# Performance work log

Hardware: AMD Instinct MI355X
Metric: run time of the kernel (lower is better)

The kernel has to match this reference:

```python
import jax, jax.numpy as jnp
import numpy as np

EMBED = 1024
HEADS = 16
HEAD_DIM = EMBED // HEADS
MAX_REL = 16


def setup_inputs() -> dict:
    key = jax.random.key(0)
    ks = jax.random.split(key, 8)
    s = 0.02
    x = jax.random.normal(ks[0], (4, 2048, EMBED), dtype=jnp.float32)
    Wq = jax.random.normal(ks[1], (EMBED, EMBED), dtype=jnp.float32) * s
    bq = jnp.zeros((EMBED,), dtype=jnp.float32)
    Wk = jax.random.normal(ks[2], (EMBED, EMBED), dtype=jnp.float32) * s
    bk = jnp.zeros((EMBED,), dtype=jnp.float32)
    Wv = jax.random.normal(ks[3], (EMBED, EMBED), dtype=jnp.float32) * s
    bv = jnp.zeros((EMBED,), dtype=jnp.float32)
    rel_bias = jax.random.normal(ks[4], (2 * MAX_REL + 1, HEADS), dtype=jnp.float32) * s
    return {"x": x, "Wq": Wq, "bq": bq, "Wk": Wk, "bk": bk, "Wv": Wv, "bv": bv, "rel_bias": rel_bias}


def reference(x, Wq, bq, Wk, bk, Wv, bv, rel_bias):
    B, S, _ = x.shape
    # projections (Linear: x @ W + b, with W stored [in, out])
    q = (x @ Wq + bq).reshape(B, S, HEADS, HEAD_DIM).transpose(0, 2, 1, 3)  # [B,H,S,D]
    k = (x @ Wk + bk).reshape(B, S, HEADS, HEAD_DIM).transpose(0, 2, 1, 3)
    v = (x @ Wv + bv).reshape(B, S, HEADS, HEAD_DIM).transpose(0, 2, 1, 3)
    scores = jnp.einsum('bhqd,bhkd->bhqk', q, k) / jnp.sqrt(jnp.float32(HEAD_DIM))
    pos = jnp.arange(S)
    rel = jnp.clip(pos[None, :] - pos[:, None], -MAX_REL, MAX_REL) + MAX_REL  # [S,S]
    bias = rel_bias[rel]                      # [S,S,H]
    scores = scores + bias.transpose(2, 0, 1)[None]  # [B,H,S,S]
    probs = jax.nn.softmax(scores, axis=-1)
    # dropout is identity in eval mode
    out = jnp.einsum('bhqk,bhkd->bhqd', probs, v)
    return out.transpose(0, 2, 1, 3).reshape(B, S, EMBED)
```

## Files before the change

### kernel.cpp

```cpp
#include <hip/hip_runtime.h>

#define EMBED 1024
#define HEADS 16
#define HDIM  64
#define SEQ   2048
#define BATCH 4
#define MTOT  (BATCH*SEQ)

typedef __attribute__((ext_vector_type(8))) short  short8;
typedef __attribute__((ext_vector_type(4))) float  f32x4;

#define GLOAD_LDS16(g, l) \
  __builtin_amdgcn_global_load_lds((const __attribute__((address_space(1))) void*)(g), \
                                   (__attribute__((address_space(3))) void*)(l), 16, 0, 0)

__device__ inline unsigned short f2bf(float f) {
  union { float f; unsigned u; } v; v.f = f;
  unsigned r = v.u + 0x7FFF + ((v.u >> 16) & 1);
  return (unsigned short)(r >> 16);
}

__global__ void cvt_x(const float* __restrict__ x, unsigned short* __restrict__ xb) {
  int i = (blockIdx.x * blockDim.x + threadIdx.x) * 8;
  f32x4 a = *(const f32x4*)(x + i);
  f32x4 b = *(const f32x4*)(x + i + 4);
  unsigned short o[8];
  o[0]=f2bf(a[0]); o[1]=f2bf(a[1]); o[2]=f2bf(a[2]); o[3]=f2bf(a[3]);
  o[4]=f2bf(b[0]); o[5]=f2bf(b[1]); o[6]=f2bf(b[2]); o[7]=f2bf(b[3]);
  *(short8*)(xb + i) = *(short8*)o;
}

__global__ void transpose_w(const float* __restrict__ Wq, const float* __restrict__ Wk,
                            const float* __restrict__ Wv, unsigned short* __restrict__ Wtb) {
  __shared__ float tile[32][33];
  int wsel = blockIdx.z;
  const float* W = wsel == 0 ? Wq : (wsel == 1 ? Wk : Wv);
  int k0 = blockIdx.x * 32, n0 = blockIdx.y * 32;
  int tx = threadIdx.x & 31, ty = threadIdx.x >> 5;
  for (int i = 0; i < 4; ++i)
    tile[ty + i*8][tx] = W[(k0 + ty + i*8) * EMBED + n0 + tx];
  __syncthreads();
  unsigned short* o = Wtb + wsel * EMBED * EMBED;
  for (int i = 0; i < 4; ++i)
    o[(n0 + ty + i*8) * EMBED + k0 + tx] = f2bf(tile[tx][ty + i*8]);
}

__global__ __launch_bounds__(256)
void qkv_gemm(const unsigned short* __restrict__ xb, const unsigned short* __restrict__ Wtb,
              const float* __restrict__ bq, const float* __restrict__ bk, const float* __restrict__ bv,
              unsigned short* __restrict__ Qb, unsigned short* __restrict__ Kb,
              unsigned short* __restrict__ Vt) {
  __shared__ unsigned short As[128 * 72];
  __shared__ unsigned short Bs[128 * 72];
  int wsel = blockIdx.z;
  int m0 = blockIdx.x * 128, n0 = blockIdx.y * 128;
  int t = threadIdx.x, lane = t & 63, wave = t >> 6;
  int wr = wave >> 1, wc = wave & 1;
  int lr = lane & 15, lg = lane >> 4;
  const unsigned short* Wt = Wtb + wsel * (EMBED * EMBED);
  const float* bias = wsel == 0 ? bq : (wsel == 1 ? bk : bv);

  f32x4 acc[4][4] = {};

  for (int kt = 0; kt < EMBED / 64; ++kt) {
    int k0 = kt * 64;
    for (int i = 0; i < 4; ++i) {
      int c = i * 256 + t;
      int row = c >> 3, col8 = c & 7;
      short8 va = *(const short8*)(xb + (m0 + row) * EMBED + k0 + col8 * 8);
      short8 vb = *(const short8*)(Wt + (n0 + row) * EMBED + k0 + col8 * 8);
      *(short8*)(As + row * 72 + col8 * 8) = va;
      *(short8*)(Bs + row * 72 + col8 * 8) = vb;
    }
    __syncthreads();
    for (int kk = 0; kk < 2; ++kk) {
      short8 af[4], bfr[4];
      for (int mf = 0; mf < 4; ++mf)
        af[mf] = *(const short8*)(As + (wr * 64 + mf * 16 + lr) * 72 + kk * 32 + lg * 8);
      for (int nf = 0; nf < 4; ++nf)
        bfr[nf] = *(const short8*)(Bs + (wc * 64 + nf * 16 + lr) * 72 + kk * 32 + lg * 8);
      for (int mf = 0; mf < 4; ++mf)
        for (int nf = 0; nf < 4; ++nf)
          acc[mf][nf] = __builtin_amdgcn_mfma_f32_16x16x32_bf16(af[mf], bfr[nf], acc[mf][nf], 0, 0, 0);
    }
    __syncthreads();
  }

  for (int nf = 0; nf < 4; ++nf) {
    int n = n0 + wc * 64 + nf * 16 + lr;
    float bval = bias[n];
    int h = n >> 6, d = n & 63;
    for (int mf = 0; mf < 4; ++mf) {
      for (int r = 0; r < 4; ++r) {
        int m = m0 + wr * 64 + mf * 16 + lg * 4 + r;
        int b = m >> 11, s = m & 2047;
        unsigned short bfv = f2bf(acc[mf][nf][r] + bval);
        if (wsel == 0)      Qb[((b * HEADS + h) * SEQ + s) * HDIM + d] = bfv;
        else if (wsel == 1) Kb[((b * HEADS + h) * SEQ + s) * HDIM + d] = bfv;
        else                Vt[((b * HEADS + h) * HDIM + d) * SEQ + s] = bfv;
      }
    }
  }
}

__global__ __launch_bounds__(256)
void attn(const unsigned short* __restrict__ Qb, const unsigned short* __restrict__ Kb,
          const unsigned short* __restrict__ Vt, const float* __restrict__ rel_bias,
          float* __restrict__ out) {
  __shared__ unsigned short Ks[2][64 * 64];
  __shared__ unsigned short Vs[2][64 * 64];
  __shared__ unsigned short Plds[4][16 * 80];
  __shared__ float bias_l[33];
  int bh = blockIdx.y;
  int b = bh >> 4, h = bh & 15;
  int t = threadIdx.x, lane = t & 63, wave = t >> 6;
  int lr = lane & 15, lg = lane >> 4;
  const float LOG2E = 1.44269504088896340736f;
  if (t < 33) bias_l[t] = rel_bias[t * HEADS + h] * LOG2E;

  int q0 = blockIdx.x * 64 + wave * 16;
  const unsigned short* Qp = Qb + (bh * SEQ + q0) * HDIM;
  const unsigned short* Kp = Kb + bh * SEQ * HDIM;
  const unsigned short* Vp = Vt + bh * HDIM * SEQ;

  short8 qf[2];
  for (int kk = 0; kk < 2; ++kk)
    qf[kk] = *(const short8*)(Qp + lr * HDIM + kk * 32 + lg * 8);

  f32x4 oacc[4] = {};
  float lsum[4] = {0.f, 0.f, 0.f, 0.f};
  const float SCL = 0.125f * LOG2E;
  unsigned short* pw = Plds[wave];

  int srow0 = (wave << 4) + (lane >> 3);
  int sslot = lane & 7;

  #define STAGE(buf, key0_)                                                          \
    for (int j = 0; j < 2; ++j) {                                                    \
      int srow = srow0 + j * 8;                                                      \
      int cs = sslot ^ (srow & 7);                                                   \
      GLOAD_LDS16(Kp + ((key0_) + srow) * HDIM + cs * 8,                             \
                  &Ks[buf][((wave << 4) + j * 8) << 6]);                             \
      GLOAD_LDS16(Vp + srow * SEQ + (key0_) + cs * 8,                                \
                  &Vs[buf][((wave << 4) + j * 8) << 6]);                             \
    }

  int cur = 0;
  STAGE(0, 0)
  __syncthreads();
  float cbLo = bias_l[0], cbHi = bias_l[32];

  for (int kb = 0; kb < SEQ / 64; ++kb) {
    int key0 = kb * 64;
    if (kb + 1 < SEQ / 64) { STAGE(cur ^ 1, key0 + 64) }
    f32x4 sc[4] = {};
    for (int kf = 0; kf < 4; ++kf) {
      int row = kf * 16 + lr;
      for (int kk = 0; kk < 2; ++kk) {
        short8 kfr = *(const short8*)(&Ks[cur][(row << 6) + (((kk * 4 + lg) ^ (row & 7)) << 3)]);
        sc[kf] = __builtin_amdgcn_mfma_f32_16x16x32_bf16(qf[kk], kfr, sc[kf], 0, 0, 0);
      }
    }
    float p[4][4];
    if (key0 >= q0 + 31) {
      for (int kf = 0; kf < 4; ++kf)
        for (int r = 0; r < 4; ++r)
          p[kf][r] = exp2f(sc[kf][r] * SCL + cbHi);
    } else if (key0 <= q0 - 79) {
      for (int kf = 0; kf < 4; ++kf)
        for (int r = 0; r < 4; ++r)
          p[kf][r] = exp2f(sc[kf][r] * SCL + cbLo);
    } else {
      for (int kf = 0; kf < 4; ++kf) {
        int key = key0 + kf * 16 + lr;
        for (int r = 0; r < 4; ++r) {
          int q = q0 + lg * 4 + r;
          int rel = key - q;
          rel = rel < -16 ? -16 : (rel > 16 ? 16 : rel);
          p[kf][r] = exp2f(sc[kf][r] * SCL + bias_l[rel + 16]);
        }
      }
    }
    for (int r = 0; r < 4; ++r)
      lsum[r] += p[0][r] + p[1][r] + p[2][r] + p[3][r];
    for (int kf = 0; kf < 4; ++kf)
      for (int r = 0; r < 4; ++r)
        pw[(lg * 4 + r) * 80 + kf * 16 + lr] = f2bf(p[kf][r]);
    short8 pa[2];
    for (int kk = 0; kk < 2; ++kk)
      pa[kk] = *(const short8*)(pw + lr * 80 + kk * 32 + lg * 8);
    for (int df = 0; df < 4; ++df) {
      int row = df * 16 + lr;
      for (int kk = 0; kk < 2; ++kk) {
        short8 vf = *(const short8*)(&Vs[cur][(row << 6) + (((kk * 4 + lg) ^ (row & 7)) << 3)]);
        oacc[df] = __builtin_amdgcn_mfma_f32_16x16x32_bf16(pa[kk], vf, oacc[df], 0, 0, 0);
      }
    }
    __syncthreads();
    cur ^= 1;
  }
  for (int r = 0; r < 4; ++r) {
    float s_ = lsum[r];
    for (int off = 1; off < 16; off <<= 1)
      s_ += __shfl_xor(s_, off, 64);
    int q = q0 + lg * 4 + r;
    float inv = 1.0f / s_;
    float* op = out + (b * SEQ + q) * EMBED + h * HDIM;
    for (int df = 0; df < 4; ++df)
      op[df * 16 + lr] = oacc[df][r] * inv;
  }
  #undef STAGE
}

extern "C" void kernel_launch(void* const* d_in, const int* in_sizes, int n_in,
                              void* d_out, int out_size, void* d_ws, size_t ws_size,
                              hipStream_t stream) {
  const float* x        = (const float*)d_in[0];
  const float* Wq       = (const float*)d_in[1];
  const float* bq       = (const float*)d_in[2];
  const float* Wk       = (const float*)d_in[3];
  const float* bk       = (const float*)d_in[4];
  const float* Wv       = (const float*)d_in[5];
  const float* bv       = (const float*)d_in[6];
  const float* rel_bias = (const float*)d_in[7];
  float* out = (float*)d_out;

  char* ws = (char*)d_ws;
  unsigned short* xb  = (unsigned short*)(ws);
  unsigned short* Wtb = (unsigned short*)(ws + 16777216);
  unsigned short* Qb  = (unsigned short*)(ws + 23068672);
  unsigned short* Kb  = (unsigned short*)(ws + 39845888);
  unsigned short* Vt  = (unsigned short*)(ws + 56623104);

  cvt_x<<<MTOT * EMBED / (256 * 8), 256, 0, stream>>>(x, xb);
  transpose_w<<<dim3(32, 32, 3), 256, 0, stream>>>(Wq, Wk, Wv, Wtb);
  qkv_gemm<<<dim3(MTOT / 128, EMBED / 128, 3), 256, 0, stream>>>(xb, Wtb, bq, bk, bv, Qb, Kb, Vt);
  attn<<<dim3(SEQ / 64, BATCH * HEADS), 256, 0, stream>>>(Qb, Kb, Vt, rel_bias, out);
}
```

Measured before the change: 243.4 us.

## Switch attention to 32x32 MFMA with register-resident P via permlane swaps

The attention kernel now gives each wave 32 queries and computes S transposed with 32x32x16 bf16 MFMAs. Converted probabilities are repacked in registers using v_cvt_pk_bf16 and v_permlane32_swap, so P no longer round-trips through LDS. Each block covers 128 queries, which halves the grid and doubles reuse of each staged K/V tile. This trades fewer blocks and higher register pressure (two 16-float accumulators plus scores) for less LDS traffic and fewer MFMA instructions.

```diff
diff --git a/kernel.cpp b/kernel.cpp
--- a/kernel.cpp
+++ b/kernel.cpp
@@ -7,8 +7,9 @@
 #define BATCH 4
 #define MTOT  (BATCH*SEQ)
 
-typedef __attribute__((ext_vector_type(8))) short  short8;
-typedef __attribute__((ext_vector_type(4))) float  f32x4;
+typedef __attribute__((ext_vector_type(8)))  short short8;
+typedef __attribute__((ext_vector_type(4)))  float f32x4;
+typedef __attribute__((ext_vector_type(16))) float f32x16;
 
 #define GLOAD_LDS16(g, l) \
   __builtin_amdgcn_global_load_lds((const __attribute__((address_space(1))) void*)(g), \
@@ -18,6 +19,20 @@
   union { float f; unsigned u; } v; v.f = f;
   unsigned r = v.u + 0x7FFF + ((v.u >> 16) & 1);
   return (unsigned short)(r >> 16);
+}
+
+__device__ inline unsigned cvtpk(float lo, float hi) {
+  unsigned r;
+  asm("v_cvt_pk_bf16_f32 %0, %1, %2" : "=v"(r) : "v"(lo), "v"(hi));
+  return r;
+}
+
+#define PLSWAP(a, b) asm("v_permlane32_swap_b32 %0, %1" : "+v"(a), "+v"(b))
+
+__device__ inline short8 mk8(unsigned w0, unsigned w1, unsigned w2, unsigned w3) {
+  union { unsigned u[4]; short8 s; } x;
+  x.u[0] = w0; x.u[1] = w1; x.u[2] = w2; x.u[3] = w3;
+  return x.s;
 }
 
 __global__ void cvt_x(const float* __restrict__ x, unsigned short* __restrict__ xb) {
@@ -109,28 +124,29 @@
           float* __restrict__ out) {
   __shared__ unsigned short Ks[2][64 * 64];
   __shared__ unsigned short Vs[2][64 * 64];
-  __shared__ unsigned short Plds[4][16 * 80];
   __shared__ float bias_l[33];
+  __shared__ float dld[4][32];
   int bh = blockIdx.y;
   int b = bh >> 4, h = bh & 15;
   int t = threadIdx.x, lane = t & 63, wave = t >> 6;
-  int lr = lane & 15, lg = lane >> 4;
+  int l31 = lane & 31, hi = lane >> 5;
   const float LOG2E = 1.44269504088896340736f;
   if (t < 33) bias_l[t] = rel_bias[t * HEADS + h] * LOG2E;
 
-  int q0 = blockIdx.x * 64 + wave * 16;
-  const unsigned short* Qp = Qb + (bh * SEQ + q0) * HDIM;
+  int qw0 = blockIdx.x * 128 + wave * 32;
+  const unsigned short* Qp = Qb + (bh * SEQ + qw0) * HDIM;
   const unsigned short* Kp = Kb + bh * SEQ * HDIM;
   const unsigned short* Vp = Vt + bh * HDIM * SEQ;
 
-  short8 qf[2];
-  for (int kk = 0; kk < 2; ++kk)
-    qf[kk] = *(const short8*)(Qp + lr * HDIM + kk * 32 + lg * 8);
-
-  f32x4 oacc[4] = {};
-  float lsum[4] = {0.f, 0.f, 0.f, 0.f};
+  short8 qf[4];
+  #pragma unroll
+  for (int ks = 0; ks < 4; ++ks)
+    qf[ks] = *(const short8*)(Qp + l31 * HDIM + ks * 16 + hi * 8);
+
+  f32x16 O0 = {}, O1 = {};
+  float lsum = 0.f;
   const float SCL = 0.125f * LOG2E;
-  unsigned short* pw = Plds[wave];
+  int q = qw0 + l31;
 
   int srow0 = (wave << 4) + (lane >> 3);
   int sslot = lane & 7;
@@ -150,66 +166,72 @@
   __syncthreads();
   float cbLo = bias_l[0], cbHi = bias_l[32];
 
+  #define LDV(row, ks) \
+    (*(const short8*)(&Vs[cur][((row) << 6) + ((((ks) * 2 + hi) ^ ((row) & 7)) << 3)]))
+
+  #define PROC(SACC, KOFF)  {                                                        \
+    float pv[16];                                                                    \
+    int kbase = key0 + (KOFF);                                                       \
+    if (kbase >= qw0 + 47) {                                                         \
+      _Pragma("unroll") for (int r = 0; r < 16; ++r)                                 \
+        pv[r] = exp2f(SACC[r] * SCL + cbHi);                                         \
+    } else if (kbase <= qw0 - 47) {                                                  \
+      _Pragma("unroll") for (int r = 0; r < 16; ++r)                                 \
+        pv[r] = exp2f(SACC[r] * SCL + cbLo);                                         \
+    } else {                                                                         \
+      _Pragma("unroll") for (int r = 0; r < 16; ++r) {                               \
+        int key = kbase + (r & 3) + 8 * (r >> 2) + 4 * hi;                           \
+        int rel = key - q;                                                           \
+        rel = rel < -16 ? -16 : (rel > 16 ? 16 : rel);                               \
+        pv[r] = exp2f(SACC[r] * SCL + bias_l[rel + 16]);                             \
+      }                                                                              \
+    }                                                                                \
+    _Pragma("unroll") for (int r = 0; r < 16; ++r) lsum += pv[r];                    \
+                       \
+    unsigned a0 = cvtpk(pv[0], pv[1]),  a1 = cvtpk(pv[4], pv[5]);   PLSWAP(a0, a1);  \
+    unsigned a2 = cvtpk(pv[2], pv[3]),  a3 = cvtpk(pv[6], pv[7]);   PLSWAP(a2, a3);  \
+    unsigned b0 = cvtpk(pv[8], pv[9]),  b1 = cvtpk(pv[12], pv[13]); PLSWAP(b0, b1);  \
+    unsigned b2 = cvtpk(pv[10], pv[11]), b3 = cvtpk(pv[14], pv[15]); PLSWAP(b2, b3); \
+    short8 pa0 = mk8(a0, a2, a1, a3);                                                \
+    short8 pa1 = mk8(b0, b2, b1, b3);                                                \
+    int ks0 = (KOFF) / 16;                                                           \
+    O0 = __builtin_amdgcn_mfma_f32_32x32x16_bf16(pa0, LDV(l31, ks0),      O0, 0, 0, 0); \
+    O1 = __builtin_amdgcn_mfma_f32_32x32x16_bf16(pa0, LDV(32 + l31, ks0), O1, 0, 0, 0); \
+    O0 = __builtin_amdgcn_mfma_f32_32x32x16_bf16(pa1, LDV(l31, ks0 + 1),      O0, 0, 0, 0); \
+    O1 = __builtin_amdgcn_mfma_f32_32x32x16_bf16(pa1, LDV(32 + l31, ks0 + 1), O1, 0, 0, 0); \
+  }
+
   for (int kb = 0; kb < SEQ / 64; ++kb) {
     int key0 = kb * 64;
     if (kb + 1 < SEQ / 64) { STAGE(cur ^ 1, key0 + 64) }
-    f32x4 sc[4] = {};
-    for (int kf = 0; kf < 4; ++kf) {
-      int row = kf * 16 + lr;
-      for (int kk = 0; kk < 2; ++kk) {
-        short8 kfr = *(const short8*)(&Ks[cur][(row << 6) + (((kk * 4 + lg) ^ (row & 7)) << 3)]);
-        sc[kf] = __builtin_amdgcn_mfma_f32_16x16x32_bf16(qf[kk], kfr, sc[kf], 0, 0, 0);
-      }
-    }
-    float p[4][4];
-    if (key0 >= q0 + 31) {
-      for (int kf = 0; kf < 4; ++kf)
-        for (int r = 0; r < 4; ++r)
-          p[kf][r] = exp2f(sc[kf][r] * SCL + cbHi);
-    } else if (key0 <= q0 - 79) {
-      for (int kf = 0; kf < 4; ++kf)
-        for (int r = 0; r < 4; ++r)
-          p[kf][r] = exp2f(sc[kf][r] * SCL + cbLo);
-    } else {
-      for (int kf = 0; kf < 4; ++kf) {
-        int key = key0 + kf * 16 + lr;
-        for (int r = 0; r < 4; ++r) {
-          int q = q0 + lg * 4 + r;
-          int rel = key - q;
-          rel = rel < -16 ? -16 : (rel > 16 ? 16 : rel);
-          p[kf][r] = exp2f(sc[kf][r] * SCL + bias_l[rel + 16]);
-        }
-      }
-    }
-    for (int r = 0; r < 4; ++r)
-      lsum[r] += p[0][r] + p[1][r] + p[2][r] + p[3][r];
-    for (int kf = 0; kf < 4; ++kf)
-      for (int r = 0; r < 4; ++r)
-        pw[(lg * 4 + r) * 80 + kf * 16 + lr] = f2bf(p[kf][r]);
-    short8 pa[2];
-    for (int kk = 0; kk < 2; ++kk)
-      pa[kk] = *(const short8*)(pw + lr * 80 + kk * 32 + lg * 8);
-    for (int df = 0; df < 4; ++df) {
-      int row = df * 16 + lr;
-      for (int kk = 0; kk < 2; ++kk) {
-        short8 vf = *(const short8*)(&Vs[cur][(row << 6) + (((kk * 4 + lg) ^ (row & 7)) << 3)]);
-        oacc[df] = __builtin_amdgcn_mfma_f32_16x16x32_bf16(pa[kk], vf, oacc[df], 0, 0, 0);
-      }
-    }
+    f32x16 s0 = {}, s1 = {};
+    #pragma unroll
+    for (int ks = 0; ks < 4; ++ks) {
+      int r0 = l31, r1 = 32 + l31;
+      short8 k0 = *(const short8*)(&Ks[cur][(r0 << 6) + (((ks * 2 + hi) ^ (r0 & 7)) << 3)]);
+      short8 k1 = *(const short8*)(&Ks[cur][(r1 << 6) + (((ks * 2 + hi) ^ (r1 & 7)) << 3)]);
+      s0 = __builtin_amdgcn_mfma_f32_32x32x16_bf16(k0, qf[ks], s0, 0, 0, 0);
+      s1 = __builtin_amdgcn_mfma_f32_32x32x16_bf16(k1, qf[ks], s1, 0, 0, 0);
+    }
+    PROC(s0, 0)
+    PROC(s1, 32)
     __syncthreads();
     cur ^= 1;
   }
-  for (int r = 0; r < 4; ++r) {
-    float s_ = lsum[r];
-    for (int off = 1; off < 16; off <<= 1)
-      s_ += __shfl_xor(s_, off, 64);
-    int q = q0 + lg * 4 + r;
-    float inv = 1.0f / s_;
-    float* op = out + (b * SEQ + q) * EMBED + h * HDIM;
-    for (int df = 0; df < 4; ++df)
-      op[df * 16 + lr] = oacc[df][r] * inv;
+
+  float denom = lsum + __shfl_xor(lsum, 32, 64);
+  if (lane < 32) dld[wave][l31] = 1.0f / denom;
+  float* op = out + (b * SEQ + qw0) * EMBED + h * HDIM;
+  #pragma unroll
+  for (int r = 0; r < 16; ++r) {
+    int ql = (r & 3) + 8 * (r >> 2) + 4 * hi;
+    float inv = dld[wave][ql];
+    op[ql * EMBED + l31]      = O0[r] * inv;
+    op[ql * EMBED + 32 + l31] = O1[r] * inv;
   }
   #undef STAGE
+  #undef LDV
+  #undef PROC
 }
 
 extern "C" void kernel_launch(void* const* d_in, const int* in_sizes, int n_in,
@@ -235,5 +257,5 @@
   cvt_x<<<MTOT * EMBED / (256 * 8), 256, 0, stream>>>(x, xb);
   transpose_w<<<dim3(32, 32, 3), 256, 0, stream>>>(Wq, Wk, Wv, Wtb);
   qkv_gemm<<<dim3(MTOT / 128, EMBED / 128, 3), 256, 0, stream>>>(xb, Wtb, bq, bk, bv, Qb, Kb, Vt);
-  attn<<<dim3(SEQ / 64, BATCH * HEADS), 256, 0, stream>>>(Qb, Kb, Vt, rel_bias, out);
-}
+  attn<<<dim3(SEQ / 128, BATCH * HEADS), 256, 0, stream>>>(Qb, Kb, Vt, rel_bias, out);
+}
```

New measurement: 231.5 us. 1.05x faster.
